# Optimization experiments

Measured on AMD Instinct MI355X. Metric: run time of the kernel, lower is better.

Reference implementation:

```python
import jax, jax.numpy as jnp
import numpy as np


def setup_inputs() -> dict:
    key = jax.random.key(0)
    ks = jax.random.split(key, 7)
    B, T, D, H = 32, 512, 512, 512
    return {
        "x": jax.random.normal(ks[0], (B, T, D), dtype=jnp.float32),
        "W_Du": jax.random.normal(ks[1], (D, H), dtype=jnp.float32) * (1.0 / np.sqrt(D)),
        "W_Dr1": jax.random.normal(ks[2], (D, H), dtype=jnp.float32) * (1.0 / np.sqrt(D)),
        "W_Dr2": jax.random.normal(ks[3], (D, H), dtype=jnp.float32) * (1.0 / np.sqrt(D)),
        "b_Du": jax.random.normal(ks[4], (H,), dtype=jnp.float32) * 0.02,
        "b_Dr1": jax.random.normal(ks[5], (H,), dtype=jnp.float32) * 0.02,
        "b_Dr2": jax.random.normal(ks[6], (H,), dtype=jnp.float32) * 0.02,
    }


def reference(x, W_Du, W_Dr1, W_Dr2, b_Du, b_Dr1, b_Dr2):
    # Precompute all per-step projections across time (batched matmuls),
    # then run the strictly sequential gated recurrence with lax.scan.
    r1 = jax.nn.softmax(jnp.einsum('btd,dh->bth', x, W_Dr1) + b_Dr1, axis=-1)  # [B,T,H]
    r2 = jax.nn.softmax(jnp.einsum('btd,dh->bth', x, W_Dr2) + b_Dr2, axis=-1)  # [B,T,H]
    u = jnp.tanh(jnp.einsum('btd,dh->bth', x, W_Du) + b_Du)                     # [B,T,H]

    def step(s, inp):
        r1t, r2t, ut = inp
        s_new = r1t * s + r2t * ut
        return s_new, s_new

    init = jnp.zeros((x.shape[0], W_Du.shape[1]), dtype=x.dtype)
    # time-major for scan: [T,B,H]
    _, ys = jax.lax.scan(
        step, init,
        (jnp.swapaxes(r1, 0, 1), jnp.swapaxes(r2, 0, 1), jnp.swapaxes(u, 0, 1)),
    )
    return jnp.swapaxes(ys, 0, 1)  # [B,T,H]
```

## Files before the change

kernel.cpp:

```cpp
#include <hip/hip_runtime.h>
#include <hip/hip_bf16.h>

#define B_N 32
#define T_N 512
#define D_N 512
#define H_N 512
#define M_N (B_N * T_N)

typedef __attribute__((ext_vector_type(8))) short bf16x8;
typedef __attribute__((ext_vector_type(4))) float f32x4;

__device__ __forceinline__ unsigned short f2bf(float f) {
  unsigned u = __float_as_uint(f);
  u += 0x7FFFu + ((u >> 16) & 1u);
  return (unsigned short)(u >> 16);
}
__device__ __forceinline__ unsigned short f2h(float f) {
  _Float16 h = (_Float16)f;
  return *(unsigned short*)&h;
}
__device__ __forceinline__ float h2f(unsigned short u) {
  _Float16 h = *(_Float16*)&u;
  return (float)h;
}

#define GLOAD16(g, l) __builtin_amdgcn_global_load_lds( \
    (const __attribute__((address_space(1))) void*)(g), \
    (__attribute__((address_space(3))) void*)(l), 16, 0, 0)

__global__ void prep_kernel(const float* __restrict__ x,
                            const float* __restrict__ W0,
                            const float* __restrict__ W1,
                            const float* __restrict__ W2,
                            unsigned short* __restrict__ xb,
                            unsigned short* __restrict__ Wt,
                            float* __restrict__ S) {
  int blk = blockIdx.x;
  int tid = threadIdx.x;
  if (blk < 768) {
    __shared__ float tile[32][33];
    int id = blk >> 8;
    int t = blk & 255;
    int kr = (t >> 4) << 5;
    int nc = (t & 15) << 5;
    const float* W = (id == 0) ? W0 : (id == 1) ? W1 : W2;
    unsigned short* Wo = Wt + (size_t)id * (D_N * H_N);
    int tx = tid & 31, ty0 = tid >> 5;
    for (int ty = ty0; ty < 32; ty += 8)
      tile[ty][tx] = W[(size_t)(kr + ty) * H_N + nc + tx];
    __syncthreads();
    for (int ty = ty0; ty < 32; ty += 8)
      Wo[(size_t)(nc + ty) * D_N + kr + tx] = f2bf(tile[tx][ty]);
  } else if (blk < 2816) {
    int b = blk - 768;
    const float4* xv = (const float4*)x;
#pragma unroll
    for (int u = 0; u < 4; ++u) {
      int i = b * 1024 + u * 256 + tid;
      float4 v = xv[i];
      ushort4 o;
      o.x = f2bf(v.x); o.y = f2bf(v.y); o.z = f2bf(v.z); o.w = f2bf(v.w);
      ((ushort4*)xb)[i] = o;
    }
  } else {
    ((float4*)S)[(blk - 2816) * 256 + tid] = (float4){0.f, 0.f, 0.f, 0.f};
  }
}

__global__ __launch_bounds__(256) void gemm3(
    const unsigned short* __restrict__ xb,
    const unsigned short* __restrict__ Wt,
    const float* __restrict__ bDu,
    const float* __restrict__ bDr1,
    const float* __restrict__ bDr2,
    unsigned short* __restrict__ uP,
    unsigned short* __restrict__ e1P,
    unsigned short* __restrict__ e2P,
    float* __restrict__ S1,
    float* __restrict__ S2) {
  __shared__ __align__(16) char smem[65536];

  const int wg = (blockIdx.x & 7) * 192 + (blockIdx.x >> 3);
  const int bx = wg / 12;
  const int rzy = wg - bx * 12;
  const int id = rzy >> 2;
  const int by = rzy & 3;

  const int tid = threadIdx.x;
  const int lane = tid & 63;
  const int wv = tid >> 6;
  const int wr = wv >> 1;
  const int wc = wv & 1;
  const int g = lane >> 4;
  const int c16 = lane & 15;

  const int m0 = bx * 128;
  const int n0 = by * 128;
  const unsigned short* Wp = Wt + (size_t)id * (D_N * H_N);

  f32x4 acc[4][4];
#pragma unroll
  for (int mt = 0; mt < 4; ++mt)
#pragma unroll
    for (int nt = 0; nt < 4; ++nt)
      acc[mt][nt] = (f32x4){0.f, 0.f, 0.f, 0.f};

  const int rowoff = tid >> 3;
  const int lsl = ((tid & 7) ^ ((tid >> 3) & 7)) * 8;
  const unsigned short* aSrc = xb + (size_t)(m0 + rowoff) * D_N + lsl;
  const unsigned short* bSrc = Wp + (size_t)(n0 + rowoff) * D_N + lsl;
  const int dstOff = wv * 1024;

  const int h3 = c16 & 7;

#define STAGE(buf, kstep) do {                                           \
    const int k0_ = (kstep) * 64;                                        \
    _Pragma("unroll")                                                    \
    for (int i = 0; i < 4; ++i)                                          \
      GLOAD16(aSrc + (size_t)i * (32 * D_N) + k0_,                       \
              smem + (buf) * 16384 + dstOff + i * 4096);                 \
    _Pragma("unroll")                                                    \
    for (int i = 0; i < 4; ++i)                                          \
      GLOAD16(bSrc + (size_t)i * (32 * D_N) + k0_,                       \
              smem + 32768 + (buf) * 16384 + dstOff + i * 4096);         \
  } while (0)

#define COMPUTE(buf) do {                                                \
    _Pragma("unroll")                                                    \
    for (int kh = 0; kh < 2; ++kh) {                                     \
      const int soff = ((kh * 4 + g) ^ h3) << 4;                         \
      bf16x8 af[4], bb[4];                                               \
      _Pragma("unroll")                                                  \
      for (int mt = 0; mt < 4; ++mt)                                     \
        af[mt] = *(const bf16x8*)(smem + (buf) * 16384 +                 \
                                  (wr * 64 + mt * 16 + c16) * 128 + soff); \
      _Pragma("unroll")                                                  \
      for (int nt = 0; nt < 4; ++nt)                                     \
        bb[nt] = *(const bf16x8*)(smem + 32768 + (buf) * 16384 +         \
                                  (wc * 64 + nt * 16 + c16) * 128 + soff); \
      _Pragma("unroll")                                                  \
      for (int mt = 0; mt < 4; ++mt)                                     \
        _Pragma("unroll")                                                \
        for (int nt = 0; nt < 4; ++nt)                                   \
          acc[mt][nt] = __builtin_amdgcn_mfma_f32_16x16x32_bf16(         \
              af[mt], bb[nt], acc[mt][nt], 0, 0, 0);                     \
    }                                                                    \
  } while (0)

  STAGE(0, 0);
  __syncthreads();
#pragma unroll 1
  for (int t = 0; t < 8; ++t) {
    const int buf = t & 1;
    if (t < 7) STAGE(buf ^ 1, t + 1);
    COMPUTE(buf);
    __syncthreads();
  }

  const float* bp = (id == 0) ? bDu : (id == 1) ? bDr1 : bDr2;
  unsigned short* outp = (id == 0) ? uP : (id == 1) ? e1P : e2P;
  float* Sp = (id == 1) ? S1 : S2;
  float bias[4];
#pragma unroll
  for (int nt = 0; nt < 4; ++nt)
    bias[nt] = bp[n0 + wc * 64 + nt * 16 + c16];

#pragma unroll
  for (int mt = 0; mt < 4; ++mt)
#pragma unroll
    for (int i = 0; i < 4; ++i) {
      int row = m0 + wr * 64 + mt * 16 + g * 4 + i;
      unsigned short* op = outp + (size_t)row * H_N + n0 + wc * 64 + c16;
      if (id == 0) {
#pragma unroll
        for (int nt = 0; nt < 4; ++nt) {
          float z = acc[mt][nt][i] + bias[nt];
          float e = __expf(2.f * z);
          op[nt * 16] = f2h(1.f - 2.f * __builtin_amdgcn_rcpf(e + 1.f));
        }
      } else {
        float ps = 0.f;
#pragma unroll
        for (int nt = 0; nt < 4; ++nt) {
          float e = __expf(acc[mt][nt][i] + bias[nt]);
          op[nt * 16] = f2h(e);
          ps += e;
        }
        ps += __shfl_xor(ps, 1);
        ps += __shfl_xor(ps, 2);
        ps += __shfl_xor(ps, 4);
        ps += __shfl_xor(ps, 8);
        if (c16 == 0) atomicAdd(&Sp[row], ps);
      }
    }
#undef STAGE
#undef COMPUTE
}

__global__ void scan_pass1(const unsigned short* __restrict__ e1P,
                           const unsigned short* __restrict__ e2P,
                           const unsigned short* __restrict__ uP,
                           const float* __restrict__ S1,
                           const float* __restrict__ S2,
                           float* __restrict__ cP,
                           float* __restrict__ cS) {
  __shared__ float ls1[64], ls2[64];
  int gt = blockIdx.x * 256 + threadIdx.x;
  int chunk = gt >> 14;
  int r = gt & 16383;
  int b = r >> 9, h = r & 511;
  int row0 = b * T_N + chunk * 64;
  if (threadIdx.x < 64) ls1[threadIdx.x] = 1.f / S1[row0 + threadIdx.x];
  else if (threadIdx.x < 128) ls2[threadIdx.x - 64] = 1.f / S2[row0 + threadIdx.x - 64];
  __syncthreads();
  size_t idx = (size_t)row0 * H_N + h;
  float p = 1.f, s = 0.f;
#pragma unroll 4
  for (int j = 0; j < 64; ++j) {
    float a = ls1[j] * h2f(e1P[idx]);
    float cu = ls2[j] * h2f(e2P[idx]) * h2f(uP[idx]);
    s = fmaf(a, s, cu);
    p *= a;
    idx += H_N;
  }
  cP[gt] = p;
  cS[gt] = s;
}

__global__ void scan_pass3(const unsigned short* __restrict__ e1P,
                           const unsigned short* __restrict__ e2P,
                           const unsigned short* __restrict__ uP,
                           const float* __restrict__ S1,
                           const float* __restrict__ S2,
                           const float* __restrict__ cP,
                           const float* __restrict__ cS,
                           float* __restrict__ out) {
  __shared__ float ls1[64], ls2[64];
  int gt = blockIdx.x * 256 + threadIdx.x;
  int chunk = gt >> 14;
  int r = gt & 16383;
  int b = r >> 9, h = r & 511;
  int row0 = b * T_N + chunk * 64;
  if (threadIdx.x < 64) ls1[threadIdx.x] = 1.f / S1[row0 + threadIdx.x];
  else if (threadIdx.x < 128) ls2[threadIdx.x - 64] = 1.f / S2[row0 + threadIdx.x - 64];
  float s = 0.f;
  for (int c2 = 0; c2 < chunk; ++c2)
    s = fmaf(cP[c2 * 16384 + r], s, cS[c2 * 16384 + r]);
  __syncthreads();
  size_t idx = (size_t)row0 * H_N + h;
#pragma unroll 4
  for (int j = 0; j < 64; ++j) {
    float a = ls1[j] * h2f(e1P[idx]);
    float cu = ls2[j] * h2f(e2P[idx]) * h2f(uP[idx]);
    s = fmaf(a, s, cu);
    out[idx] = s;
    idx += H_N;
  }
}

extern "C" void kernel_launch(void* const* d_in, const int* in_sizes, int n_in,
                              void* d_out, int out_size, void* d_ws, size_t ws_size,
                              hipStream_t stream) {
  const float* x  = (const float*)d_in[0];
  const float* W0 = (const float*)d_in[1];
  const float* W1 = (const float*)d_in[2];
  const float* W2 = (const float*)d_in[3];
  const float* b0 = (const float*)d_in[4];
  const float* b1 = (const float*)d_in[5];
  const float* b2 = (const float*)d_in[6];
  float* out = (float*)d_out;

  char* ws = (char*)d_ws;
  unsigned short* xb  = (unsigned short*)ws;
  unsigned short* Wt  = (unsigned short*)(ws + 16777216);
  unsigned short* uP  = (unsigned short*)(ws + 18350080);
  unsigned short* e1P = (unsigned short*)(ws + 35127296);
  unsigned short* e2P = (unsigned short*)(ws + 51904512);
  float*          S1  = (float*)(ws + 68681728);
  float*          S2  = (float*)(ws + 68747264);
  float*          cP  = (float*)(ws + 68812800);
  float*          cS  = (float*)(ws + 69337088);

  prep_kernel<<<2848, 256, 0, stream>>>(x, W0, W1, W2, xb, Wt, S1);
  gemm3<<<1536, 256, 0, stream>>>(xb, Wt, b0, b1, b2, uP, e1P, e2P, S1, S2);
  scan_pass1<<<512, 256, 0, stream>>>(e1P, e2P, uP, S1, S2, cP, cS);
  scan_pass3<<<512, 256, 0, stream>>>(e1P, e2P, uP, S1, S2, cP, cS, out);
}
```

Baseline: 82.22 us.

## Single-buffer GEMM LDS and raise occupancy to four blocks per CU

Replaces the double-buffered 64KB LDS staging in the fused projection GEMM with a single 32KB buffer, loads then syncs then computes each K step, and adds a launch bound of four blocks per SM. It also loads the A fragments one row tile at a time to lower register pressure. The aim is to hide latency through more resident workgroups instead of software prefetch. In exchange, global loads no longer overlap MFMA work within a block, and the register cap may cause spills.

```diff
diff --git a/kernel.cpp b/kernel.cpp
--- a/kernel.cpp
+++ b/kernel.cpp
@@ -67,7 +67,7 @@
   }
 }
 
-__global__ __launch_bounds__(256) void gemm3(
+__global__ __launch_bounds__(256, 4) void gemm3(
     const unsigned short* __restrict__ xb,
     const unsigned short* __restrict__ Wt,
     const float* __restrict__ bDu,
@@ -78,7 +78,7 @@
     unsigned short* __restrict__ e2P,
     float* __restrict__ S1,
     float* __restrict__ S2) {
-  __shared__ __align__(16) char smem[65536];
+  __shared__ __align__(16) char smem[32768];
 
   const int wg = (blockIdx.x & 7) * 192 + (blockIdx.x >> 3);
   const int bx = wg / 12;
@@ -113,47 +113,35 @@
 
   const int h3 = c16 & 7;
 
-#define STAGE(buf, kstep) do {                                           \
-    const int k0_ = (kstep) * 64;                                        \
-    _Pragma("unroll")                                                    \
-    for (int i = 0; i < 4; ++i)                                          \
-      GLOAD16(aSrc + (size_t)i * (32 * D_N) + k0_,                       \
-              smem + (buf) * 16384 + dstOff + i * 4096);                 \
-    _Pragma("unroll")                                                    \
-    for (int i = 0; i < 4; ++i)                                          \
-      GLOAD16(bSrc + (size_t)i * (32 * D_N) + k0_,                       \
-              smem + 32768 + (buf) * 16384 + dstOff + i * 4096);         \
-  } while (0)
-
-#define COMPUTE(buf) do {                                                \
-    _Pragma("unroll")                                                    \
-    for (int kh = 0; kh < 2; ++kh) {                                     \
-      const int soff = ((kh * 4 + g) ^ h3) << 4;                         \
-      bf16x8 af[4], bb[4];                                               \
-      _Pragma("unroll")                                                  \
-      for (int mt = 0; mt < 4; ++mt)                                     \
-        af[mt] = *(const bf16x8*)(smem + (buf) * 16384 +                 \
-                                  (wr * 64 + mt * 16 + c16) * 128 + soff); \
-      _Pragma("unroll")                                                  \
-      for (int nt = 0; nt < 4; ++nt)                                     \
-        bb[nt] = *(const bf16x8*)(smem + 32768 + (buf) * 16384 +         \
-                                  (wc * 64 + nt * 16 + c16) * 128 + soff); \
-      _Pragma("unroll")                                                  \
-      for (int mt = 0; mt < 4; ++mt)                                     \
-        _Pragma("unroll")                                                \
-        for (int nt = 0; nt < 4; ++nt)                                   \
-          acc[mt][nt] = __builtin_amdgcn_mfma_f32_16x16x32_bf16(         \
-              af[mt], bb[nt], acc[mt][nt], 0, 0, 0);                     \
-    }                                                                    \
-  } while (0)
-
-  STAGE(0, 0);
-  __syncthreads();
 #pragma unroll 1
   for (int t = 0; t < 8; ++t) {
-    const int buf = t & 1;
-    if (t < 7) STAGE(buf ^ 1, t + 1);
-    COMPUTE(buf);
+    const int k0 = t * 64;
+#pragma unroll
+    for (int i = 0; i < 4; ++i)
+      GLOAD16(aSrc + (size_t)i * (32 * D_N) + k0, smem + dstOff + i * 4096);
+#pragma unroll
+    for (int i = 0; i < 4; ++i)
+      GLOAD16(bSrc + (size_t)i * (32 * D_N) + k0,
+              smem + 16384 + dstOff + i * 4096);
+    __syncthreads();
+#pragma unroll
+    for (int kh = 0; kh < 2; ++kh) {
+      const int soff = ((kh * 4 + g) ^ h3) << 4;
+      bf16x8 bb[4];
+#pragma unroll
+      for (int nt = 0; nt < 4; ++nt)
+        bb[nt] = *(const bf16x8*)(smem + 16384 +
+                                  (wc * 64 + nt * 16 + c16) * 128 + soff);
+#pragma unroll
+      for (int mt = 0; mt < 4; ++mt) {
+        bf16x8 af = *(const bf16x8*)(smem +
+                                     (wr * 64 + mt * 16 + c16) * 128 + soff);
+#pragma unroll
+        for (int nt = 0; nt < 4; ++nt)
+          acc[mt][nt] = __builtin_amdgcn_mfma_f32_16x16x32_bf16(
+              af, bb[nt], acc[mt][nt], 0, 0, 0);
+      }
+    }
     __syncthreads();
   }
 
@@ -193,8 +181,6 @@
         if (c16 == 0) atomicAdd(&Sp[row], ps);
       }
     }
-#undef STAGE
-#undef COMPUTE
 }
 
 __global__ void scan_pass1(const unsigned short* __restrict__ e1P,
```

Result: no change. 81.64 us (-0.7%).
